# Kernel tuning notes

Measured on AMD Instinct MI355X. Metric: run time of the kernel, lower is better.

The kernel has to match this reference:

```python
import math
import jax, jax.numpy as jnp
import numpy as np

B, S, D, H = 2, 2048, 2048, 16
HD = D // H
SCALE = 1.0 / math.sqrt(HD)


def setup_inputs() -> dict:
    key = jax.random.key(0)
    kx, kq, kk, kv, ko = jax.random.split(key, 5)
    w_std = 1.0 / math.sqrt(D)
    return {
        "x": jax.random.normal(kx, (B, S, D), jnp.float32),
        "Wq": jax.random.normal(kq, (D, D), jnp.float32) * w_std,
        "Wk": jax.random.normal(kk, (D, D), jnp.float32) * w_std,
        "Wv": jax.random.normal(kv, (D, D), jnp.float32) * w_std,
        "Wo": jax.random.normal(ko, (D, D), jnp.float32) * w_std,
        "attention_mask": jnp.ones((B, S), jnp.int32),
        "sliding_window": 512,
        "sink_tokens": 4,
    }


def reference(x, Wq, Wk, Wv, Wo, attention_mask, sliding_window, sink_tokens):
    b, s, d = x.shape
    # nn.Linear(bias=False): y = x @ W^T
    q = (x @ Wq.T).reshape(b, s, H, HD).transpose(0, 2, 1, 3)  # [b,h,s,hd]
    k = (x @ Wk.T).reshape(b, s, H, HD).transpose(0, 2, 1, 3)
    v = (x @ Wv.T).reshape(b, s, H, HD).transpose(0, 2, 1, 3)

    scores = jnp.einsum("bhqd,bhkd->bhqk", q, k) * SCALE  # [b,h,s,s]

    i = jnp.arange(s)[:, None]
    j = jnp.arange(s)[None, :]
    causal = j <= i
    window = (j >= i - sliding_window + 1) & (j <= i)
    # sink mask in the source fills [0:i+1] for every row (rows < sink_tokens
    # and rows >= sink_tokens alike), i.e. it is identical to the causal mask.
    sink = causal
    allowed = causal & window & sink  # [s,s]
    pad = (attention_mask != 0)[:, None, None, :]  # [b,1,1,s]
    scores = jnp.where(allowed[None, None] & pad, scores, -jnp.inf)

    attn = jax.nn.softmax(scores, axis=-1)
    out = jnp.einsum("bhqk,bhkd->bhqd", attn, v)  # [b,h,s,hd]
    out = out.transpose(0, 2, 1, 3).reshape(b, s, d)
    return out @ Wo.T
```

## Files before the change

kernel.cpp:

```cpp
#include <hip/hip_runtime.h>
#include <stdint.h>


typedef __attribute__((ext_vector_type(8))) short short8;
typedef __attribute__((ext_vector_type(4))) float f32x4;

#define DEV static __device__ __forceinline__

DEV unsigned short f2bf(float f) {
  unsigned u = __builtin_bit_cast(unsigned, f);
  u += 0x7fffu + ((u >> 16) & 1u);
  return (unsigned short)(u >> 16);
}

DEV void async16(const void* g, void* l) {
  __builtin_amdgcn_global_load_lds(
      (const __attribute__((address_space(1))) unsigned int*)g,
      (__attribute__((address_space(3))) unsigned int*)l, 16, 0, 0);
}

__global__ __launch_bounds__(256) void cast_all(
    const float* __restrict__ x, const float* __restrict__ Wq,
    const float* __restrict__ Wk, const float* __restrict__ Wv,
    const float* __restrict__ Wo, unsigned short* __restrict__ xb,
    unsigned short* __restrict__ wqkv, unsigned short* __restrict__ wob) {
  const int bid = blockIdx.x;
  const float* src;
  unsigned short* dst;
  int i;
  if (bid < 4096) {
    src = x; dst = xb; i = bid * 256 + threadIdx.x;
  } else if (bid < 6144) {
    src = Wq; dst = wqkv; i = (bid - 4096) * 256 + threadIdx.x;
  } else if (bid < 8192) {
    src = Wk; dst = wqkv + 4194304; i = (bid - 6144) * 256 + threadIdx.x;
  } else if (bid < 10240) {
    src = Wv; dst = wqkv + 8388608; i = (bid - 8192) * 256 + threadIdx.x;
  } else {
    src = Wo; dst = wob; i = (bid - 10240) * 256 + threadIdx.x;
  }
  const float4* s4 = (const float4*)src;
  float4 a = s4[2 * (size_t)i], b = s4[2 * (size_t)i + 1];
  short8 o;
  o[0] = (short)f2bf(a.x); o[1] = (short)f2bf(a.y);
  o[2] = (short)f2bf(a.z); o[3] = (short)f2bf(a.w);
  o[4] = (short)f2bf(b.x); o[5] = (short)f2bf(b.y);
  o[6] = (short)f2bf(b.z); o[7] = (short)f2bf(b.w);
  *(short8*)(dst + 8 * (size_t)i) = o;
}

constexpr int GK = 2048, GN = 2048;

template <bool STORE_BF16>
__global__ __launch_bounds__(256) void gemm_bt(
    const unsigned short* __restrict__ A, const unsigned short* __restrict__ B,
    void* __restrict__ Cout, size_t obuf_stride) {
  __shared__ short As[128 * 32];
  __shared__ short Bs[128 * 32];
  const int t = threadIdx.x;
  const int wave = t >> 6, lane = t & 63;
  const int row0 = blockIdx.x * 128;
  const int col0g = blockIdx.y * 128;
  const int nb = col0g >> 11, col0 = col0g & 2047;
  const int wrow = (wave >> 1) * 64, wcol = (wave & 1) * 64;

  f32x4 acc[4][4] = {};

  const int srow = wave * 16 + (lane >> 2);
  const int cg = (lane & 3) ^ (lane >> 4);
  const unsigned short* Ag0 = A + (size_t)(row0 + srow) * GK + cg * 8;
  const unsigned short* Ag1 = A + (size_t)(row0 + 64 + srow) * GK + cg * 8;
  const unsigned short* Bg0 = B + (size_t)(col0g + srow) * GK + cg * 8;
  const unsigned short* Bg1 = B + (size_t)(col0g + 64 + srow) * GK + cg * 8;
  char* lA0 = (char*)As + wave * 1024;
  char* lA1 = (char*)As + 4096 + wave * 1024;
  char* lB0 = (char*)Bs + wave * 1024;
  char* lB1 = (char*)Bs + 4096 + wave * 1024;

  const int quad = lane >> 4, l15 = lane & 15;
  const int cpos = quad ^ ((l15 >> 2) & 3);
  const short* ap[4];
  const short* bp[4];
#pragma unroll
  for (int i = 0; i < 4; ++i) {
    ap[i] = As + (wrow + i * 16 + l15) * 32 + cpos * 8;
    bp[i] = Bs + (wcol + i * 16 + l15) * 32 + cpos * 8;
  }

  for (int kk = 0; kk < GK; kk += 32) {
    async16(Ag0 + kk, lA0);
    async16(Ag1 + kk, lA1);
    async16(Bg0 + kk, lB0);
    async16(Bg1 + kk, lB1);
    __syncthreads();
    short8 af[4], bf[4];
#pragma unroll
    for (int i = 0; i < 4; ++i) af[i] = *(const short8*)ap[i];
#pragma unroll
    for (int i = 0; i < 4; ++i) bf[i] = *(const short8*)bp[i];
#pragma unroll
    for (int mi = 0; mi < 4; ++mi)
#pragma unroll
      for (int ni = 0; ni < 4; ++ni)
        acc[mi][ni] = __builtin_amdgcn_mfma_f32_16x16x32_bf16(
            af[mi], bf[ni], acc[mi][ni], 0, 0, 0);
    __syncthreads();
  }

#pragma unroll
  for (int mi = 0; mi < 4; ++mi)
#pragma unroll
    for (int ni = 0; ni < 4; ++ni)
#pragma unroll
      for (int r = 0; r < 4; ++r) {
        int row = row0 + wrow + mi * 16 + quad * 4 + r;
        int col = col0 + wcol + ni * 16 + l15;
        if (STORE_BF16)
          ((unsigned short*)Cout)[nb * obuf_stride + (size_t)row * GN + col] =
              f2bf(acc[mi][ni][r]);
        else
          ((float*)Cout)[nb * obuf_stride + (size_t)row * GN + col] =
              acc[mi][ni][r];
      }
}

__global__ __launch_bounds__(256) void transpose_v(
    const unsigned short* __restrict__ vb, unsigned short* __restrict__ vtb) {
  __shared__ unsigned short tile[64][72];
  const int s0 = blockIdx.x * 64, d0 = blockIdx.y * 64, b = blockIdx.z;
  const int tid = threadIdx.x;
  const int c8 = tid & 7;
#pragma unroll
  for (int i = 0; i < 2; ++i) {
    int row = i * 32 + (tid >> 3);
    uint4 v = *(const uint4*)(vb + (size_t)(b * 2048 + s0 + row) * 2048 + d0 + c8 * 8);
    *(uint4*)&tile[row][c8 * 8] = v;
  }
  __syncthreads();
#pragma unroll
  for (int i = 0; i < 2; ++i) {
    int dr = i * 32 + (tid >> 3);
    short8 sv;
#pragma unroll
    for (int j = 0; j < 8; ++j) sv[j] = (short)tile[c8 * 8 + j][dr];
    int d = d0 + dr;
    int h = d >> 7, hd = d & 127;
    *(short8*)(vtb + ((size_t)(b * 16 + h) * 128 + hd) * 2048 + s0 + c8 * 8) = sv;
  }
}

__global__ __launch_bounds__(256, 3) void attn_mfma(
    const unsigned short* __restrict__ Qm, const unsigned short* __restrict__ Km,
    const unsigned short* __restrict__ Vt, unsigned short* __restrict__ Om,
    const int* __restrict__ amask, const int* __restrict__ winp) {
  constexpr int S = 2048, D = 2048, HD = 128;
  const float SCALE = 0.08838834764831845f;

  __shared__ short Ks[64 * 128];
  __shared__ short Vts[128 * 64];
  __shared__ short Ps[4][16 * 64];

  const int t = threadIdx.x, w = t >> 6, lane = t & 63;
  const int quad = lane >> 4, l15 = lane & 15;
  const int l7 = l15 & 7;
  const int f = blockIdx.x;
  const int qt = f >> 5, g = f & 31;
  const int h = g & 15, b = g >> 4;
  const int qi0 = qt * 64;
  const int win = winp[0];

  short8 qf[4];
  {
    const unsigned short* qp =
        Qm + (size_t)(b * S + qi0 + w * 16 + l15) * D + h * HD + quad * 8;
#pragma unroll
    for (int kc = 0; kc < 4; ++kc) qf[kc] = *(const short8*)(qp + kc * 32);
  }

  f32x4 o[8] = {};
  float m_r[4], l_r[4];
#pragma unroll
  for (int r = 0; r < 4; ++r) { m_r[r] = -1e30f; l_r[r] = 0.f; }

  int lowj = qi0 - win + 1;
  if (lowj < 0) lowj = 0;
  const int jt0 = lowj >> 6;

  const int krow = lane >> 4, kpos = lane & 15;
  const int vrow = lane >> 3, vpos = lane & 7;

  for (int jt = jt0; jt <= qt; ++jt) {
    const int j0 = jt * 64;
    __syncthreads();
#pragma unroll
    for (int ii = 0; ii < 4; ++ii) {
      int row = ii * 16 + w * 4 + krow;
      int c = kpos ^ (row & 7);
      async16(Km + (size_t)(b * S + j0 + row) * D + h * HD + c * 8,
              (char*)Ks + (ii * 16 + w * 4) * 256);
    }
#pragma unroll
    for (int ii = 0; ii < 4; ++ii) {
      int row = ii * 32 + w * 8 + vrow;
      int c = vpos ^ (row & 7);
      async16(Vt + ((size_t)(b * 16 + h) * 128 + row) * S + j0 + c * 8,
              (char*)Vts + (ii * 32 + w * 8) * 128);
    }
    __syncthreads();

    f32x4 sS[4];
#pragma unroll
    for (int ni = 0; ni < 4; ++ni) {
      f32x4 acc = {0.f, 0.f, 0.f, 0.f};
#pragma unroll
      for (int kc = 0; kc < 4; ++kc) {
        int pos = (kc * 4 + quad) ^ l7;
        short8 bk = *(const short8*)&Ks[(ni * 16 + l15) * 128 + pos * 8];
        acc = __builtin_amdgcn_mfma_f32_16x16x32_bf16(qf[kc], bk, acc, 0, 0, 0);
      }
      sS[ni] = acc;
    }

    float sv[4][4];
    int amv[4];
#pragma unroll
    for (int ni = 0; ni < 4; ++ni) amv[ni] = amask[b * S + j0 + ni * 16 + l15];
#pragma unroll
    for (int ni = 0; ni < 4; ++ni)
#pragma unroll
      for (int r = 0; r < 4; ++r) {
        int gi = qi0 + w * 16 + quad * 4 + r;
        int gj = j0 + ni * 16 + l15;
        bool ok = (gj <= gi) && (gj >= gi - win + 1) && (amv[ni] != 0);
        sv[ni][r] = ok ? sS[ni][r] * SCALE : -1e30f;
      }
    float alpha[4], mnew[4];
#pragma unroll
    for (int r = 0; r < 4; ++r) {
      float mx = fmaxf(fmaxf(sv[0][r], sv[1][r]), fmaxf(sv[2][r], sv[3][r]));
      mx = fmaxf(mx, __shfl_xor(mx, 1));
      mx = fmaxf(mx, __shfl_xor(mx, 2));
      mx = fmaxf(mx, __shfl_xor(mx, 4));
      mx = fmaxf(mx, __shfl_xor(mx, 8));
      float mn = fmaxf(m_r[r], mx);
      alpha[r] = __expf(m_r[r] - mn);
      m_r[r] = mn;
      mnew[r] = mn;
    }
    float rs[4] = {0.f, 0.f, 0.f, 0.f};
#pragma unroll
    for (int ni = 0; ni < 4; ++ni)
#pragma unroll
      for (int r = 0; r < 4; ++r) {
        float p = (sv[ni][r] > -1e29f) ? __expf(sv[ni][r] - mnew[r]) : 0.f;
        sv[ni][r] = p;
        rs[r] += p;
      }
#pragma unroll
    for (int r = 0; r < 4; ++r) {
      float s = rs[r];
      s += __shfl_xor(s, 1);
      s += __shfl_xor(s, 2);
      s += __shfl_xor(s, 4);
      s += __shfl_xor(s, 8);
      l_r[r] = l_r[r] * alpha[r] + s;
    }
#pragma unroll
    for (int ni = 0; ni < 4; ++ni)
#pragma unroll
      for (int r = 0; r < 4; ++r) {
        int row = quad * 4 + r;
        int col = ni * 16 + l15;
        int pos = (col >> 3) ^ (row & 7);
        Ps[w][row * 64 + pos * 8 + (col & 7)] = (short)f2bf(sv[ni][r]);
      }
#pragma unroll
    for (int ni2 = 0; ni2 < 8; ++ni2)
#pragma unroll
      for (int r = 0; r < 4; ++r) o[ni2][r] *= alpha[r];

    __asm__ __volatile__("s_waitcnt lgkmcnt(0)" ::: "memory");

    short8 aP[2];
#pragma unroll
    for (int kc2 = 0; kc2 < 2; ++kc2) {
      int pos = (kc2 * 4 + quad) ^ l7;
      aP[kc2] = *(const short8*)&Ps[w][l15 * 64 + pos * 8];
    }
#pragma unroll
    for (int ni2 = 0; ni2 < 8; ++ni2) {
#pragma unroll
      for (int kc2 = 0; kc2 < 2; ++kc2) {
        int pos = (kc2 * 4 + quad) ^ l7;
        short8 bv = *(const short8*)&Vts[(ni2 * 16 + l15) * 64 + pos * 8];
        o[ni2] = __builtin_amdgcn_mfma_f32_16x16x32_bf16(aP[kc2], bv, o[ni2], 0, 0, 0);
      }
    }
  }

  float inv[4];
#pragma unroll
  for (int r = 0; r < 4; ++r) inv[r] = 1.f / l_r[r];
#pragma unroll
  for (int ni2 = 0; ni2 < 8; ++ni2)
#pragma unroll
    for (int r = 0; r < 4; ++r) {
      int row = qi0 + w * 16 + quad * 4 + r;
      Om[(size_t)(b * S + row) * D + h * HD + ni2 * 16 + l15] =
          f2bf(o[ni2][r] * inv[r]);
    }
}

extern "C" void kernel_launch(void* const* d_in, const int* in_sizes, int n_in,
                              void* d_out, int out_size, void* d_ws,
                              size_t ws_size, hipStream_t stream) {
  (void)in_sizes; (void)n_in; (void)out_size; (void)ws_size;
  const float* x  = (const float*)d_in[0];
  const float* Wq = (const float*)d_in[1];
  const float* Wk = (const float*)d_in[2];
  const float* Wv = (const float*)d_in[3];
  const float* Wo = (const float*)d_in[4];
  const int* am   = (const int*)d_in[5];
  const int* win  = (const int*)d_in[6];

  char* ws = (char*)d_ws;
  unsigned short* xb   = (unsigned short*)(ws + 0);
  unsigned short* vtb  = (unsigned short*)(ws + 0);
  unsigned short* wqkv = (unsigned short*)(ws + 16777216);
  unsigned short* wob  = (unsigned short*)(ws + 41943040);
  unsigned short* qb   = (unsigned short*)(ws + 50331648);
  unsigned short* kb   = (unsigned short*)(ws + 67108864);
  unsigned short* vb   = (unsigned short*)(ws + 83886080);
  unsigned short* ab   = (unsigned short*)(ws + 100663296);

  cast_all<<<dim3(12288), dim3(256), 0, stream>>>(x, Wq, Wk, Wv, Wo, xb, wqkv, wob);

  gemm_bt<true><<<dim3(32, 48), dim3(256), 0, stream>>>(xb, wqkv, qb, 8388608);

  transpose_v<<<dim3(32, 32, 2), dim3(256), 0, stream>>>(vb, vtb);

  attn_mfma<<<dim3(1024), dim3(256), 0, stream>>>(qb, kb, vtb, ab, am, win);

  gemm_bt<false><<<dim3(32, 16), dim3(256), 0, stream>>>(ab, wob, d_out, 0);
}
```

Measured before the change: 364.8 us.

## Rewrite GEMM as 8-wave 128x256 tile with triple-buffered async loads

```diff
diff --git a/kernel.cpp b/kernel.cpp
--- a/kernel.cpp
+++ b/kernel.cpp
@@ -51,60 +51,122 @@
 
 constexpr int GK = 2048, GN = 2048;
 
+#define GEMM_PHASE(ni_)                                                     \
+  __builtin_amdgcn_s_setprio(1);                                            \
+  {                                                                         \
+    _Pragma("unroll") for (int mi = 0; mi < 4; ++mi) {                      \
+      acc[mi][ni_] = __builtin_amdgcn_mfma_f32_16x16x32_bf16(               \
+          af[mi][0], bfr[ni_][0], acc[mi][ni_], 0, 0, 0);                   \
+      acc[mi][ni_] = __builtin_amdgcn_mfma_f32_16x16x32_bf16(               \
+          af[mi][1], bfr[ni_][1], acc[mi][ni_], 0, 0, 0);                   \
+    }                                                                       \
+  }                                                                         \
+  __builtin_amdgcn_s_setprio(0);
+
 template <bool STORE_BF16>
-__global__ __launch_bounds__(256) void gemm_bt(
+__global__ __launch_bounds__(512, 2) void gemm_bt8(
     const unsigned short* __restrict__ A, const unsigned short* __restrict__ B,
     void* __restrict__ Cout, size_t obuf_stride) {
-  __shared__ short As[128 * 32];
-  __shared__ short Bs[128 * 32];
+  __shared__ short As[3][128 * 64];
+  __shared__ short Bs[3][256 * 64];
+
   const int t = threadIdx.x;
-  const int wave = t >> 6, lane = t & 63;
-  const int row0 = blockIdx.x * 128;
-  const int col0g = blockIdx.y * 128;
+  const int lane = t & 63;
+  const int quad = lane >> 4, l15 = lane & 15, l7 = l15 & 7;
+  const int w = t >> 6, wm = w >> 2, wn = w & 3;
+
+  const int nwg = (int)gridDim.x;
+  const int cpx = nwg >> 3;
+  const int swz = ((int)blockIdx.x & 7) * cpx + ((int)blockIdx.x >> 3);
+  const int bx = swz & 31;
+  const int by = swz >> 5;
+  const int row0 = bx * 128;
+  const int col0g = by * 256;
   const int nb = col0g >> 11, col0 = col0g & 2047;
-  const int wrow = (wave >> 1) * 64, wcol = (wave & 1) * 64;
+
+  const int rsub = t >> 3;
+  const int cg8 = ((t & 7) ^ (rsub & 7)) << 3;
+  const unsigned short* Ag = A + (size_t)(row0 + rsub) * GK + cg8;
+  const unsigned short* Bg = B + (size_t)(col0g + rsub) * GK + cg8;
+  const int loff = rsub * 128 + (t & 7) * 16;
+
+  auto stageA = [&](int buf, int kt) {
+    async16(Ag + (size_t)kt * 64, (char*)As[buf] + loff);
+    async16(Ag + 64 * (size_t)GK + (size_t)kt * 64,
+            (char*)As[buf] + 8192 + loff);
+  };
+  auto stageB01 = [&](int buf, int kt) {
+    async16(Bg + (size_t)kt * 64, (char*)Bs[buf] + loff);
+    async16(Bg + 64 * (size_t)GK + (size_t)kt * 64,
+            (char*)Bs[buf] + 8192 + loff);
+  };
+  auto stageB23 = [&](int buf, int kt) {
+    async16(Bg + 128 * (size_t)GK + (size_t)kt * 64,
+            (char*)Bs[buf] + 16384 + loff);
+    async16(Bg + 192 * (size_t)GK + (size_t)kt * 64,
+            (char*)Bs[buf] + 24576 + loff);
+  };
+
+  int aoff[4][2], boff[4][2];
+#pragma unroll
+  for (int mi = 0; mi < 4; ++mi)
+#pragma unroll
+    for (int kc = 0; kc < 2; ++kc)
+      aoff[mi][kc] =
+          (wm * 64 + mi * 16 + l15) * 64 + (((kc * 4 + quad) ^ l7) << 3);
+#pragma unroll
+  for (int ni = 0; ni < 4; ++ni)
+#pragma unroll
+    for (int kc = 0; kc < 2; ++kc)
+      boff[ni][kc] =
+          (wn * 64 + ni * 16 + l15) * 64 + (((kc * 4 + quad) ^ l7) << 3);
 
   f32x4 acc[4][4] = {};
-
-  const int srow = wave * 16 + (lane >> 2);
-  const int cg = (lane & 3) ^ (lane >> 4);
-  const unsigned short* Ag0 = A + (size_t)(row0 + srow) * GK + cg * 8;
-  const unsigned short* Ag1 = A + (size_t)(row0 + 64 + srow) * GK + cg * 8;
-  const unsigned short* Bg0 = B + (size_t)(col0g + srow) * GK + cg * 8;
-  const unsigned short* Bg1 = B + (size_t)(col0g + 64 + srow) * GK + cg * 8;
-  char* lA0 = (char*)As + wave * 1024;
-  char* lA1 = (char*)As + 4096 + wave * 1024;
-  char* lB0 = (char*)Bs + wave * 1024;
-  char* lB1 = (char*)Bs + 4096 + wave * 1024;
-
-  const int quad = lane >> 4, l15 = lane & 15;
-  const int cpos = quad ^ ((l15 >> 2) & 3);
-  const short* ap[4];
-  const short* bp[4];
-#pragma unroll
-  for (int i = 0; i < 4; ++i) {
-    ap[i] = As + (wrow + i * 16 + l15) * 32 + cpos * 8;
-    bp[i] = Bs + (wcol + i * 16 + l15) * 32 + cpos * 8;
-  }
-
-  for (int kk = 0; kk < GK; kk += 32) {
-    async16(Ag0 + kk, lA0);
-    async16(Ag1 + kk, lA1);
-    async16(Bg0 + kk, lB0);
-    async16(Bg1 + kk, lB1);
-    __syncthreads();
-    short8 af[4], bf[4];
-#pragma unroll
-    for (int i = 0; i < 4; ++i) af[i] = *(const short8*)ap[i];
-#pragma unroll
-    for (int i = 0; i < 4; ++i) bf[i] = *(const short8*)bp[i];
-#pragma unroll
-    for (int mi = 0; mi < 4; ++mi)
-#pragma unroll
-      for (int ni = 0; ni < 4; ++ni)
-        acc[mi][ni] = __builtin_amdgcn_mfma_f32_16x16x32_bf16(
-            af[mi], bf[ni], acc[mi][ni], 0, 0, 0);
-    __syncthreads();
+  constexpr int NT = GK / 64;
+
+  stageA(0, 0); stageB01(0, 0); stageB23(0, 0);
+  stageA(1, 1); stageB01(1, 1); stageB23(1, 1);
+  __asm__ __volatile__("s_waitcnt vmcnt(6)" ::: "memory");
+  __builtin_amdgcn_s_barrier();
+
+  int bufR = 0;
+  for (int T = 0; T < NT; ++T) {
+    const short* ab = As[bufR];
+    const short* bb = Bs[bufR];
+    int bufW = bufR + 2; if (bufW >= 3) bufW -= 3;
+
+    short8 af[4][2], bfr[4][2];
+#pragma unroll
+    for (int mi = 0; mi < 4; ++mi) {
+      af[mi][0] = *(const short8*)(ab + aoff[mi][0]);
+      af[mi][1] = *(const short8*)(ab + aoff[mi][1]);
+    }
+#pragma unroll
+    for (int ni = 0; ni < 4; ++ni) {
+      bfr[ni][0] = *(const short8*)(bb + boff[ni][0]);
+      bfr[ni][1] = *(const short8*)(bb + boff[ni][1]);
+    }
+    __builtin_amdgcn_s_barrier();
+    GEMM_PHASE(0)
+
+    if (T + 2 < NT) stageA(bufW, T + 2);
+    __builtin_amdgcn_s_barrier();
+    GEMM_PHASE(1)
+
+    if (T + 2 < NT) stageB01(bufW, T + 2);
+    __builtin_amdgcn_s_barrier();
+    GEMM_PHASE(2)
+
+    if (T + 2 < NT) stageB23(bufW, T + 2);
+    if (T < NT - 2) {
+      __asm__ __volatile__("s_waitcnt vmcnt(6)" ::: "memory");
+    } else if (T == NT - 2) {
+      __asm__ __volatile__("s_waitcnt vmcnt(0)" ::: "memory");
+    }
+    __builtin_amdgcn_s_barrier();
+    GEMM_PHASE(3)
+
+    bufR = bufR + 1 == 3 ? 0 : bufR + 1;
   }
 
 #pragma unroll
@@ -113,8 +175,8 @@
     for (int ni = 0; ni < 4; ++ni)
 #pragma unroll
       for (int r = 0; r < 4; ++r) {
-        int row = row0 + wrow + mi * 16 + quad * 4 + r;
-        int col = col0 + wcol + ni * 16 + l15;
+        int row = row0 + wm * 64 + mi * 16 + quad * 4 + r;
+        int col = col0 + wn * 64 + ni * 16 + l15;
         if (STORE_BF16)
           ((unsigned short*)Cout)[nb * obuf_stride + (size_t)row * GN + col] =
               f2bf(acc[mi][ni][r]);
@@ -335,11 +397,11 @@
 
   cast_all<<<dim3(12288), dim3(256), 0, stream>>>(x, Wq, Wk, Wv, Wo, xb, wqkv, wob);
 
-  gemm_bt<true><<<dim3(32, 48), dim3(256), 0, stream>>>(xb, wqkv, qb, 8388608);
+  gemm_bt8<true><<<dim3(768), dim3(512), 0, stream>>>(xb, wqkv, qb, 8388608);
 
   transpose_v<<<dim3(32, 32, 2), dim3(256), 0, stream>>>(vb, vtb);
 
   attn_mfma<<<dim3(1024), dim3(256), 0, stream>>>(qb, kb, vtb, ab, am, win);
 
-  gemm_bt<false><<<dim3(32, 16), dim3(256), 0, stream>>>(ab, wob, d_out, 0);
-}
+  gemm_bt8<false><<<dim3(256), dim3(512), 0, stream>>>(ab, wob, d_out, 0);
+}
```

Measured after the change: 386.5 us. +5.9%, slower.

## Replace GEMM with 256x256-tile double-buffered pipelined MFMA kernel

Applied to the files above, without the earlier changes.

```diff
diff --git a/kernel.cpp b/kernel.cpp
--- a/kernel.cpp
+++ b/kernel.cpp
@@ -51,76 +51,193 @@
 
 constexpr int GK = 2048, GN = 2048;
 
+#define MFMA_BF16 __builtin_amdgcn_mfma_f32_16x16x32_bf16
+
+#define STAGE_A(buf, h, kt)                                                  \
+  {                                                                          \
+    const unsigned short* g_ = Ag + (size_t)((h) * 128) * GK + (kt) * 64;    \
+    char* d_ = (char*)As[buf] + (h) * 16384 + loff;                          \
+    async16(g_, d_);                                                         \
+    async16(g_ + (size_t)64 * GK, d_ + 8192);                                \
+  }
+#define STAGE_B(buf, h, kt)                                                  \
+  {                                                                          \
+    const unsigned short* g_ = Bg + (size_t)((h) * 128) * GK + (kt) * 64;    \
+    char* d_ = (char*)Bs[buf] + (h) * 16384 + loff;                          \
+    async16(g_, d_);                                                         \
+    async16(g_ + (size_t)64 * GK, d_ + 8192);                                \
+  }
+
+#define READ_A(buf, mq_)                                                     \
+  _Pragma("unroll") for (int mi = 0; mi < 4; ++mi)                           \
+      _Pragma("unroll") for (int kc = 0; kc < 2; ++kc) afr[mi][kc] =         \
+      *(const short8*)(As[buf] + (mq_)*4096 + aoff[mi][kc]);
+#define READ_B01(buf)                                                        \
+  _Pragma("unroll") for (int ni = 0; ni < 2; ++ni)                           \
+      _Pragma("unroll") for (int kc = 0; kc < 2; ++kc) bfr[ni][kc] =         \
+      *(const short8*)(Bs[buf] + boff[ni][kc]);
+#define READ_B23(buf)                                                        \
+  _Pragma("unroll") for (int ni = 2; ni < 4; ++ni)                           \
+      _Pragma("unroll") for (int kc = 0; kc < 2; ++kc) bfr[ni][kc] =         \
+      *(const short8*)(Bs[buf] + boff[ni][kc]);
+
+#define PH_MFMA(mq_, nq_)                                                    \
+  __builtin_amdgcn_s_setprio(1);                                             \
+  _Pragma("unroll") for (int mi = 0; mi < 4; ++mi)                           \
+      _Pragma("unroll") for (int ni = 0; ni < 2; ++ni) {                     \
+    acc[(mq_)*4 + mi][(nq_)*2 + ni] =                                        \
+        MFMA_BF16(afr[mi][0], bfr[(nq_)*2 + ni][0],                          \
+                  acc[(mq_)*4 + mi][(nq_)*2 + ni], 0, 0, 0);                 \
+    acc[(mq_)*4 + mi][(nq_)*2 + ni] =                                        \
+        MFMA_BF16(afr[mi][1], bfr[(nq_)*2 + ni][1],                          \
+                  acc[(mq_)*4 + mi][(nq_)*2 + ni], 0, 0, 0);                 \
+  }                                                                          \
+  __builtin_amdgcn_s_setprio(0);
+
+#define BAR __builtin_amdgcn_s_barrier();
+#define LGKM0 __asm__ __volatile__("s_waitcnt lgkmcnt(0)" ::: "memory");
+#define VM(n) __asm__ __volatile__("s_waitcnt vmcnt(" #n ")" ::: "memory");
+
 template <bool STORE_BF16>
-__global__ __launch_bounds__(256) void gemm_bt(
+__global__ __launch_bounds__(512, 2) void gemm256(
     const unsigned short* __restrict__ A, const unsigned short* __restrict__ B,
     void* __restrict__ Cout, size_t obuf_stride) {
-  __shared__ short As[128 * 32];
-  __shared__ short Bs[128 * 32];
+  __shared__ short As[2][16384];
+  __shared__ short Bs[2][16384];
+
   const int t = threadIdx.x;
-  const int wave = t >> 6, lane = t & 63;
-  const int row0 = blockIdx.x * 128;
-  const int col0g = blockIdx.y * 128;
+  const int lane = t & 63;
+  const int quad = lane >> 4, l15 = lane & 15, l7 = l15 & 7;
+  const int w = t >> 6, wm = w >> 2, wn = w & 3;
+
+  const int nwg = (int)gridDim.x;
+  const int cpx = nwg >> 3;
+  const int swz = ((int)blockIdx.x & 7) * cpx + ((int)blockIdx.x >> 3);
+  const int bx = swz & 15, by = swz >> 4;
+  const int row0 = bx * 256, col0g = by * 256;
   const int nb = col0g >> 11, col0 = col0g & 2047;
-  const int wrow = (wave >> 1) * 64, wcol = (wave & 1) * 64;
-
-  f32x4 acc[4][4] = {};
-
-  const int srow = wave * 16 + (lane >> 2);
-  const int cg = (lane & 3) ^ (lane >> 4);
-  const unsigned short* Ag0 = A + (size_t)(row0 + srow) * GK + cg * 8;
-  const unsigned short* Ag1 = A + (size_t)(row0 + 64 + srow) * GK + cg * 8;
-  const unsigned short* Bg0 = B + (size_t)(col0g + srow) * GK + cg * 8;
-  const unsigned short* Bg1 = B + (size_t)(col0g + 64 + srow) * GK + cg * 8;
-  char* lA0 = (char*)As + wave * 1024;
-  char* lA1 = (char*)As + 4096 + wave * 1024;
-  char* lB0 = (char*)Bs + wave * 1024;
-  char* lB1 = (char*)Bs + 4096 + wave * 1024;
-
-  const int quad = lane >> 4, l15 = lane & 15;
-  const int cpos = quad ^ ((l15 >> 2) & 3);
-  const short* ap[4];
-  const short* bp[4];
-#pragma unroll
-  for (int i = 0; i < 4; ++i) {
-    ap[i] = As + (wrow + i * 16 + l15) * 32 + cpos * 8;
-    bp[i] = Bs + (wcol + i * 16 + l15) * 32 + cpos * 8;
-  }
-
-  for (int kk = 0; kk < GK; kk += 32) {
-    async16(Ag0 + kk, lA0);
-    async16(Ag1 + kk, lA1);
-    async16(Bg0 + kk, lB0);
-    async16(Bg1 + kk, lB1);
-    __syncthreads();
-    short8 af[4], bf[4];
-#pragma unroll
-    for (int i = 0; i < 4; ++i) af[i] = *(const short8*)ap[i];
-#pragma unroll
-    for (int i = 0; i < 4; ++i) bf[i] = *(const short8*)bp[i];
-#pragma unroll
-    for (int mi = 0; mi < 4; ++mi)
-#pragma unroll
-      for (int ni = 0; ni < 4; ++ni)
-        acc[mi][ni] = __builtin_amdgcn_mfma_f32_16x16x32_bf16(
-            af[mi], bf[ni], acc[mi][ni], 0, 0, 0);
-    __syncthreads();
-  }
-
+
+  const int rsub = t >> 3;
+  const int cg8 = ((t & 7) ^ (rsub & 7)) << 3;
+  const unsigned short* Ag = A + (size_t)(row0 + rsub) * GK + cg8;
+  const unsigned short* Bg = B + (size_t)(col0g + rsub) * GK + cg8;
+  const int loff = rsub * 128 + (t & 7) * 16;
+
+  int aoff[4][2], boff[4][2];
 #pragma unroll
   for (int mi = 0; mi < 4; ++mi)
 #pragma unroll
+    for (int kc = 0; kc < 2; ++kc)
+      aoff[mi][kc] =
+          (wm * 128 + mi * 16 + l15) * 64 + (((kc * 4 + quad) ^ l7) << 3);
+#pragma unroll
+  for (int ni = 0; ni < 4; ++ni)
+#pragma unroll
+    for (int kc = 0; kc < 2; ++kc)
+      boff[ni][kc] =
+          (wn * 64 + ni * 16 + l15) * 64 + (((kc * 4 + quad) ^ l7) << 3);
+
+  f32x4 acc[8][4] = {};
+  short8 afr[4][2], bfr[4][2];
+
+  STAGE_A(0, 0, 0) STAGE_A(0, 1, 0)
+  STAGE_B(0, 0, 0) STAGE_B(0, 1, 0)
+  STAGE_B(1, 0, 1) STAGE_B(1, 1, 1)
+  VM(4)
+  BAR
+
+  for (int i = 0; i < 15; ++i) {
+    const int t1 = 2 * i + 1;
+    READ_A(0, 0) READ_B01(0)
+    STAGE_A(1, 0, t1)
+    BAR LGKM0
+    PH_MFMA(0, 0)
+    BAR
+    READ_B23(0)
+    STAGE_A(1, 1, t1)
+    BAR LGKM0
+    PH_MFMA(0, 1)
+    BAR
+    READ_A(0, 1)
+    STAGE_B(0, 0, t1 + 1)
+    BAR LGKM0
+    PH_MFMA(1, 0)
+    BAR
+    STAGE_B(0, 1, t1 + 1)
+    VM(4)
+    BAR
+    PH_MFMA(1, 1)
+    BAR
+    READ_A(1, 0) READ_B01(1)
+    STAGE_A(0, 0, t1 + 1)
+    BAR LGKM0
+    PH_MFMA(0, 0)
+    BAR
+    READ_B23(1)
+    STAGE_A(0, 1, t1 + 1)
+    BAR LGKM0
+    PH_MFMA(0, 1)
+    BAR
+    READ_A(1, 1)
+    STAGE_B(1, 0, t1 + 2)
+    BAR LGKM0
+    PH_MFMA(1, 0)
+    BAR
+    STAGE_B(1, 1, t1 + 2)
+    VM(4)
+    BAR
+    PH_MFMA(1, 1)
+    BAR
+  }
+
+  {
+    READ_A(0, 0) READ_B01(0)
+    STAGE_A(1, 0, 31)
+    BAR LGKM0
+    PH_MFMA(0, 0)
+    BAR
+    READ_B23(0)
+    STAGE_A(1, 1, 31)
+    BAR LGKM0
+    PH_MFMA(0, 1)
+    BAR
+    READ_A(0, 1)
+    BAR LGKM0
+    PH_MFMA(1, 0)
+    BAR
+    VM(0)
+    BAR
+    PH_MFMA(1, 1)
+    BAR
+    READ_A(1, 0) READ_B01(1)
+    BAR LGKM0
+    PH_MFMA(0, 0)
+    BAR
+    READ_B23(1)
+    BAR LGKM0
+    PH_MFMA(0, 1)
+    BAR
+    READ_A(1, 1)
+    BAR LGKM0
+    PH_MFMA(1, 0)
+    BAR
+    PH_MFMA(1, 1)
+  }
+
+#pragma unroll
+  for (int MI = 0; MI < 8; ++MI)
+#pragma unroll
     for (int ni = 0; ni < 4; ++ni)
 #pragma unroll
       for (int r = 0; r < 4; ++r) {
-        int row = row0 + wrow + mi * 16 + quad * 4 + r;
-        int col = col0 + wcol + ni * 16 + l15;
+        int row = row0 + wm * 128 + MI * 16 + quad * 4 + r;
+        int col = col0 + wn * 64 + ni * 16 + l15;
         if (STORE_BF16)
           ((unsigned short*)Cout)[nb * obuf_stride + (size_t)row * GN + col] =
-              f2bf(acc[mi][ni][r]);
+              f2bf(acc[MI][ni][r]);
         else
           ((float*)Cout)[nb * obuf_stride + (size_t)row * GN + col] =
-              acc[mi][ni][r];
+              acc[MI][ni][r];
       }
 }
 
@@ -335,11 +452,11 @@
 
   cast_all<<<dim3(12288), dim3(256), 0, stream>>>(x, Wq, Wk, Wv, Wo, xb, wqkv, wob);
 
-  gemm_bt<true><<<dim3(32, 48), dim3(256), 0, stream>>>(xb, wqkv, qb, 8388608);
+  gemm256<true><<<dim3(384), dim3(512), 0, stream>>>(xb, wqkv, qb, 8388608);
 
   transpose_v<<<dim3(32, 32, 2), dim3(256), 0, stream>>>(vb, vtb);
 
   attn_mfma<<<dim3(1024), dim3(256), 0, stream>>>(qb, kb, vtb, ab, am, win);
 
-  gemm_bt<false><<<dim3(32, 16), dim3(256), 0, stream>>>(ab, wob, d_out, 0);
-}
+  gemm256<false><<<dim3(128), dim3(512), 0, stream>>>(ab, wob, d_out, 0);
+}
```

Measured after the change: 378.8 us. 1.04x slower.

## Replace GEMM with triple-buffered 256x128 tile kernel using intra-block K-split waves

Applied to the files above, without the earlier changes.

```diff
diff --git a/kernel.cpp b/kernel.cpp
--- a/kernel.cpp
+++ b/kernel.cpp
@@ -51,76 +51,135 @@
 
 constexpr int GK = 2048, GN = 2048;
 
+#define MFMA_BF16 __builtin_amdgcn_mfma_f32_16x16x32_bf16
+
+#define MEMF __asm__ __volatile__("" ::: "memory");
+#define BARR { MEMF __builtin_amdgcn_s_barrier(); MEMF }
+#define SP1 __builtin_amdgcn_s_setprio(1);
+#define SP0 __builtin_amdgcn_s_setprio(0);
+#define LGKM0 __asm__ __volatile__("s_waitcnt lgkmcnt(0)" ::: "memory");
+#define VM(n) __asm__ __volatile__("s_waitcnt vmcnt(" #n ")" ::: "memory");
+
+#define STAGE_A1(bufidx, j, kt)                                              \
+  async16(Ag + (size_t)((j) * 64) * GK + (kt) * 64,                          \
+          (char*)As[bufidx] + (j) * 8192 + loff);
+#define STAGE_B1(bufidx, j, kt)                                              \
+  async16(Bg + (size_t)((j) * 64) * GK + (kt) * 64,                          \
+          (char*)Bs[bufidx] + (j) * 8192 + loff);
+
+#define READ_A(dst, bufidx, half)                                            \
+  _Pragma("unroll") for (int mi = 0; mi < 4; ++mi) dst[mi] =                 \
+      *(const short8*)(As[bufidx] + aoffb + ((half) * 4 + mi) * 1024);
+#define READ_B(dst, bufidx)                                                  \
+  _Pragma("unroll") for (int ni = 0; ni < 4; ++ni) dst[ni] =                 \
+      *(const short8*)(Bs[bufidx] + boffb + ni * 1024);
+
+#define MFMAH(half, A_, B_)                                                  \
+  _Pragma("unroll") for (int mi = 0; mi < 4; ++mi)                           \
+      _Pragma("unroll") for (int ni = 0; ni < 4; ++ni)                       \
+      acc[(half) * 4 + mi][ni] =                                             \
+      MFMA_BF16(A_[mi], B_[ni], acc[(half) * 4 + mi][ni], 0, 0, 0);
+
 template <bool STORE_BF16>
-__global__ __launch_bounds__(256) void gemm_bt(
+__global__ __launch_bounds__(512, 2) void gemm_ks(
     const unsigned short* __restrict__ A, const unsigned short* __restrict__ B,
     void* __restrict__ Cout, size_t obuf_stride) {
-  __shared__ short As[128 * 32];
-  __shared__ short Bs[128 * 32];
+  __shared__ short As[3][16384];
+  __shared__ short Bs[3][8192];
+
   const int t = threadIdx.x;
-  const int wave = t >> 6, lane = t & 63;
-  const int row0 = blockIdx.x * 128;
-  const int col0g = blockIdx.y * 128;
+  const int lane = t & 63;
+  const int quad = lane >> 4, l15 = lane & 15, l7 = l15 & 7;
+  const int w = t >> 6;
+  const int wk = w & 1, wn = (w >> 1) & 1, wm = w >> 2;
+
+  const int nwg = (int)gridDim.x;
+  const int cpx = nwg >> 3;
+  const int swz = ((int)blockIdx.x & 7) * cpx + ((int)blockIdx.x >> 3);
+  const int bx = swz & 15, by = swz >> 4;
+  const int row0 = bx * 256, col0g = by * 128;
   const int nb = col0g >> 11, col0 = col0g & 2047;
-  const int wrow = (wave >> 1) * 64, wcol = (wave & 1) * 64;
-
-  f32x4 acc[4][4] = {};
-
-  const int srow = wave * 16 + (lane >> 2);
-  const int cg = (lane & 3) ^ (lane >> 4);
-  const unsigned short* Ag0 = A + (size_t)(row0 + srow) * GK + cg * 8;
-  const unsigned short* Ag1 = A + (size_t)(row0 + 64 + srow) * GK + cg * 8;
-  const unsigned short* Bg0 = B + (size_t)(col0g + srow) * GK + cg * 8;
-  const unsigned short* Bg1 = B + (size_t)(col0g + 64 + srow) * GK + cg * 8;
-  char* lA0 = (char*)As + wave * 1024;
-  char* lA1 = (char*)As + 4096 + wave * 1024;
-  char* lB0 = (char*)Bs + wave * 1024;
-  char* lB1 = (char*)Bs + 4096 + wave * 1024;
-
-  const int quad = lane >> 4, l15 = lane & 15;
-  const int cpos = quad ^ ((l15 >> 2) & 3);
-  const short* ap[4];
-  const short* bp[4];
-#pragma unroll
-  for (int i = 0; i < 4; ++i) {
-    ap[i] = As + (wrow + i * 16 + l15) * 32 + cpos * 8;
-    bp[i] = Bs + (wcol + i * 16 + l15) * 32 + cpos * 8;
-  }
-
-  for (int kk = 0; kk < GK; kk += 32) {
-    async16(Ag0 + kk, lA0);
-    async16(Ag1 + kk, lA1);
-    async16(Bg0 + kk, lB0);
-    async16(Bg1 + kk, lB1);
-    __syncthreads();
-    short8 af[4], bf[4];
-#pragma unroll
-    for (int i = 0; i < 4; ++i) af[i] = *(const short8*)ap[i];
-#pragma unroll
-    for (int i = 0; i < 4; ++i) bf[i] = *(const short8*)bp[i];
-#pragma unroll
-    for (int mi = 0; mi < 4; ++mi)
-#pragma unroll
-      for (int ni = 0; ni < 4; ++ni)
-        acc[mi][ni] = __builtin_amdgcn_mfma_f32_16x16x32_bf16(
-            af[mi], bf[ni], acc[mi][ni], 0, 0, 0);
-    __syncthreads();
-  }
-
-#pragma unroll
-  for (int mi = 0; mi < 4; ++mi)
+
+  const int rsub = t >> 3;
+  const int cg8 = ((t & 7) ^ (rsub & 7)) << 3;
+  const unsigned short* Ag = A + (size_t)(row0 + rsub) * GK + cg8;
+  const unsigned short* Bg = B + (size_t)(col0g + rsub) * GK + cg8;
+  const int loff = rsub * 128 + (t & 7) * 16;
+
+  const int kchunk = ((wk * 4 + quad) ^ l7) << 3;
+  const int aoffb = (wm * 128 + l15) * 64 + kchunk;
+  const int boffb = (wn * 64 + l15) * 64 + kchunk;
+
+  f32x4 acc[8][4] = {};
+  short8 afA[4], afB[4], bc[4], bn[4];
+
+  STAGE_A1(0, 0, 0) STAGE_A1(0, 1, 0) STAGE_A1(0, 2, 0) STAGE_A1(0, 3, 0)
+  STAGE_B1(0, 0, 0) STAGE_B1(0, 1, 0)
+  STAGE_A1(1, 0, 1) STAGE_A1(1, 1, 1) STAGE_A1(1, 2, 1) STAGE_A1(1, 3, 1)
+  STAGE_B1(1, 0, 1) STAGE_B1(1, 1, 1)
+  VM(6)
+  BARR
+  READ_A(afA, 0, 0) READ_B(bc, 0)
+
+  int c0 = 0, c1 = 1, c2 = 2;
+#pragma unroll 1
+  for (int T = 0; T < 32; ++T) {
+    if (T < 30) { STAGE_A1(c2, 0, T + 2) STAGE_A1(c2, 1, T + 2) STAGE_A1(c2, 2, T + 2) }
+    BARR LGKM0
+    SP1 READ_A(afB, c0, 1) MFMAH(0, afA, bc) SP0
+    if (T < 30) { STAGE_A1(c2, 3, T + 2) STAGE_B1(c2, 0, T + 2) STAGE_B1(c2, 1, T + 2) }
+    if (T < 30) { VM(6) }
+    else if (T == 30) { VM(0) }
+    BARR LGKM0
+    SP1
+    if (T < 31) { READ_A(afA, c1, 0) READ_B(bn, c1) }
+    MFMAH(1, afB, bc)
+    SP0
+    if (T < 31) {
+#pragma unroll
+      for (int i = 0; i < 4; ++i) bc[i] = bn[i];
+    }
+    int tmp = c0; c0 = c1; c1 = c2; c2 = tmp;
+  }
+
+  LGKM0
+  BARR
+  char* mreg = (w < 6) ? ((char*)As + w * 16384)
+                       : ((char*)Bs + (w - 6) * 16384);
+  const int pw = w ^ 1;
+  char* preg = (pw < 6) ? ((char*)As + pw * 16384)
+                        : ((char*)Bs + (pw - 6) * 16384);
+  const int whalf = wk ^ 1;
+#pragma unroll
+  for (int MIh = 0; MIh < 4; ++MIh)
 #pragma unroll
     for (int ni = 0; ni < 4; ++ni)
+      *(f32x4*)(mreg + (MIh * 4 + ni) * 1024 + lane * 16) =
+          acc[whalf * 4 + MIh][ni];
+  LGKM0
+  BARR
+#pragma unroll
+  for (int MIh = 0; MIh < 4; ++MIh)
+#pragma unroll
+    for (int ni = 0; ni < 4; ++ni) {
+      f32x4 v = *(const f32x4*)(preg + (MIh * 4 + ni) * 1024 + lane * 16);
+      acc[wk * 4 + MIh][ni] += v;
+    }
+
+#pragma unroll
+  for (int MIh = 0; MIh < 4; ++MIh)
+#pragma unroll
+    for (int ni = 0; ni < 4; ++ni)
 #pragma unroll
       for (int r = 0; r < 4; ++r) {
-        int row = row0 + wrow + mi * 16 + quad * 4 + r;
-        int col = col0 + wcol + ni * 16 + l15;
+        int row = row0 + wm * 128 + (wk * 4 + MIh) * 16 + quad * 4 + r;
+        int col = col0 + wn * 64 + ni * 16 + l15;
         if (STORE_BF16)
           ((unsigned short*)Cout)[nb * obuf_stride + (size_t)row * GN + col] =
-              f2bf(acc[mi][ni][r]);
+              f2bf(acc[wk * 4 + MIh][ni][r]);
         else
           ((float*)Cout)[nb * obuf_stride + (size_t)row * GN + col] =
-              acc[mi][ni][r];
+              acc[wk * 4 + MIh][ni][r];
       }
 }
 
@@ -335,11 +394,11 @@
 
   cast_all<<<dim3(12288), dim3(256), 0, stream>>>(x, Wq, Wk, Wv, Wo, xb, wqkv, wob);
 
-  gemm_bt<true><<<dim3(32, 48), dim3(256), 0, stream>>>(xb, wqkv, qb, 8388608);
+  gemm_ks<true><<<dim3(768), dim3(512), 0, stream>>>(xb, wqkv, qb, 8388608);
 
   transpose_v<<<dim3(32, 32, 2), dim3(256), 0, stream>>>(vb, vtb);
 
   attn_mfma<<<dim3(1024), dim3(256), 0, stream>>>(qb, kb, vtb, ab, am, win);
 
-  gemm_bt<false><<<dim3(32, 16), dim3(256), 0, stream>>>(ab, wob, d_out, 0);
-}
+  gemm_ks<false><<<dim3(256), dim3(512), 0, stream>>>(ab, wob, d_out, 0);
+}
```

Result: slower. 513.5 us (+40.8%).
